# Optimization experiments

Measured on AMD Instinct MI355X. Metric: run time of the kernel, lower is better.

## Reference

```python
import jax, jax.numpy as jnp
import numpy as np

N, E = 20000, 320000
IN_DIM, CODE_DIM, HIDDEN, HEADS, NREL = 896, 768, 256, 4, 5
CH = HIDDEN // HEADS
CODE_WEIGHT = 3.0
NEG_SLOPE = 0.2


def _gat_layer(h, src, dst, W, att_src, att_dst, bias):
    # h: [N, HIDDEN]; src/dst already include self-loops. Eval mode -> no dropout.
    n = h.shape[0]
    x = (h @ W).reshape(n, HEADS, CH)                      # [N,H,C]
    a_src = (x * att_src).sum(-1)                          # [N,H]
    a_dst = (x * att_dst).sum(-1)                          # [N,H]
    alpha = jax.nn.leaky_relu(a_src[src] + a_dst[dst], NEG_SLOPE)  # [E',H]
    amax = jax.ops.segment_max(alpha, dst, num_segments=n)
    amax = jnp.where(jnp.isfinite(amax), amax, 0.0)
    ex = jnp.exp(alpha - amax[dst])
    denom = jax.ops.segment_sum(ex, dst, num_segments=n)
    coef = ex / denom[dst]                                 # segment softmax over in-neighbors
    msg = x[src] * coef[:, :, None]                        # [E',H,C]
    out = jax.ops.segment_sum(msg, dst, num_segments=n)    # [N,H,C]
    return out.reshape(n, HEADS * CH) + bias


def setup_inputs() -> dict:
    key = jax.random.key(0)
    ks = jax.random.split(key, 20)
    def glorot(k, shape):
        fan_in = shape[0]
        return jax.random.normal(k, shape, jnp.float32) / jnp.sqrt(jnp.asarray(fan_in, jnp.float32))
    inp = {
        "x": jax.random.normal(ks[0], (N, IN_DIM), jnp.float32),
        "edge_index": jax.random.randint(ks[1], (2, E), 0, N, jnp.int32),
        "edge_type": jax.random.randint(ks[2], (E,), 0, NREL, jnp.int32),
        "edge_weight": jax.random.uniform(ks[3], (E,), jnp.float32),
        "rel_emb": jax.random.normal(ks[4], (NREL, HIDDEN), jnp.float32),
        "Wp": glorot(ks[5], (IN_DIM, HIDDEN)),
        "bp": jnp.zeros((HIDDEN,), jnp.float32),
        "W1": glorot(ks[6], (HIDDEN, HIDDEN)),
        "att_src1": glorot(ks[7], (HEADS, CH)) * 0.1,
        "att_dst1": glorot(ks[8], (HEADS, CH)) * 0.1,
        "b1": jnp.zeros((HIDDEN,), jnp.float32),
        "W2": glorot(ks[9], (HIDDEN, HIDDEN)),
        "att_src2": glorot(ks[10], (HEADS, CH)) * 0.1,
        "att_dst2": glorot(ks[11], (HEADS, CH)) * 0.1,
        "b2": jnp.zeros((HIDDEN,), jnp.float32),
        "Wo": glorot(ks[12], (HIDDEN, 1)),
        "bo": jnp.zeros((1,), jnp.float32),
    }
    return inp


def reference(x, edge_index, edge_type, edge_weight, rel_emb, Wp, bp,
              W1, att_src1, att_dst1, b1, W2, att_src2, att_dst2, b2, Wo, bo):
    # feature reorder + code reweighting
    x_code = x[:, :CODE_DIM]
    x_num = x[:, CODE_DIM:]
    xc = jnp.concatenate([x_num, CODE_WEIGHT * x_code], axis=-1)
    h = jax.nn.relu(xc @ Wp + bp)                          # [N,HIDDEN]

    src, dst = edge_index[0], edge_index[1]
    # relational message + index_add scatter
    rel = rel_emb[edge_type] * edge_weight[:, None]        # [E,HIDDEN]
    msg = h[src] + rel
    h = h + jax.ops.segment_sum(msg, dst, num_segments=N)

    # GATConv adds self-loops by default
    loop = jnp.arange(N, dtype=src.dtype)
    src_sl = jnp.concatenate([src, loop])
    dst_sl = jnp.concatenate([dst, loop])

    h = _gat_layer(h, src_sl, dst_sl, W1, att_src1, att_dst1, b1)
    h = _gat_layer(h, src_sl, dst_sl, W2, att_src2, att_dst2, b2)
    score = (h @ Wo + bo)[:, 0]                            # [N]
    return score
```

## Files before the change

kernel.cpp:

```cpp
#include <hip/hip_runtime.h>
#include <hip/hip_bf16.h>

#define N_NODES 20000
#define E_EDGES 320000

typedef __attribute__((ext_vector_type(8))) short s8v;
typedef __attribute__((ext_vector_type(4))) float f4v;

__device__ __forceinline__ float lrelu(float v){ return v > 0.f ? v : 0.2f * v; }

__device__ __forceinline__ float bitf(unsigned short u){
  union { unsigned int i; float f; } v; v.i = ((unsigned int)u) << 16; return v.f;
}
__device__ __forceinline__ float4 bf4(const unsigned short* p){
  ushort4 u = *(const ushort4*)p;
  return make_float4(bitf(u.x), bitf(u.y), bitf(u.z), bitf(u.w));
}
__device__ __forceinline__ unsigned short bfhi(float v){
  union{float f; unsigned u;} a; a.f = v;
  unsigned r = a.u + 0x7FFFu + ((a.u >> 16) & 1u);
  return (unsigned short)(r >> 16);
}
__device__ __forceinline__ float bf2f(unsigned short h){
  union{unsigned u; float f;} a; a.u = ((unsigned)h) << 16; return a.f;
}
__device__ __forceinline__ void split2(float v0, float v1, unsigned& hu, unsigned& lu){
  __hip_bfloat162 h2 = __float22bfloat162_rn(make_float2(v0, v1));
  unsigned h; __builtin_memcpy(&h, &h2, 4);
  union{unsigned u; float f;} c0, c1;
  c0.u = h << 16;
  c1.u = h & 0xFFFF0000u;
  __hip_bfloat162 l2 = __float22bfloat162_rn(make_float2(v0 - c0.f, v1 - c1.f));
  unsigned l; __builtin_memcpy(&l, &l2, 4);
  hu = h; lu = l;
}

__global__ __launch_bounds__(256) void k_count(const int* __restrict__ dst, int* __restrict__ deg, int E){
  int e = blockIdx.x * 256 + threadIdx.x;
  if (e < E) atomicAdd(&deg[dst[e]], 1);
}

__global__ __launch_bounds__(256) void k_scan(const int* __restrict__ deg, int* __restrict__ off,
                                              int* __restrict__ cur, int n){
  __shared__ int part[256];
  __shared__ int base[257];
  int tid = threadIdx.x;
  int chunk = (n + 255) / 256;
  int st = tid * chunk;
  int en = st + chunk; if (en > n) en = n;
  int s = 0;
  for (int i = st; i < en; ++i) s += deg[i];
  part[tid] = s;
  __syncthreads();
  if (tid == 0){
    int a = 0;
    for (int i = 0; i < 256; ++i){ base[i] = a; a += part[i]; }
    base[256] = a;
  }
  __syncthreads();
  int a = base[tid];
  for (int i = st; i < en; ++i){ off[i] = a; cur[i] = 0; a += deg[i]; }
  if (tid == 0) off[n] = base[256];
}

__global__ __launch_bounds__(256) void k_fill(const int* __restrict__ src, const int* __restrict__ dst,
                       const int* __restrict__ ety, const float* __restrict__ ew,
                       const int* __restrict__ off, int* __restrict__ cur,
                       int* __restrict__ csrc, int* __restrict__ cet, float* __restrict__ cw, int E){
  int e = blockIdx.x * 256 + threadIdx.x;
  if (e < E){
    int d = dst[e];
    int p = atomicAdd(&cur[d], 1);
    int i = off[d] + p;
    csrc[i] = src[e];
    cet[i]  = ety[e];
    cw[i]   = ew[e];
  }
}

__global__ __launch_bounds__(64) void k_prep(const float* __restrict__ W, unsigned short* __restrict__ Bp, int K){
  int kt = blockIdx.x;
  int n  = blockIdx.y * 64 + threadIdx.x;
  unsigned short hi[32], lo[32];
#pragma unroll
  for (int kk = 0; kk < 32; ++kk){
    float v = W[(size_t)(kt * 32 + kk) * 256 + n];
    unsigned short h = bfhi(v);
    hi[kk] = h;
    lo[kk] = bfhi(v - bf2f(h));
  }
  size_t plane = (size_t)(K >> 5) * 256 * 32;
  size_t b = ((size_t)kt * 256 + n) * 32;
#pragma unroll
  for (int kk = 0; kk < 32; ++kk){
    Bp[b + kk]         = hi[kk];
    Bp[plane + b + kk] = lo[kk];
  }
}

template<int KT, bool PERM, bool EPI, bool ATT, bool CBF>
__global__ __launch_bounds__(128, 4) void k_mm(
    const float* __restrict__ A, const unsigned short* __restrict__ Bp,
    const float* __restrict__ bias, void* __restrict__ Cout,
    const float* __restrict__ attS, const float* __restrict__ attD,
    float* __restrict__ aS, float* __restrict__ aD, int M)
{
  constexpr int K = KT * 32;
  __shared__ unsigned short AhB[2][32 * 40];
  __shared__ unsigned short AlB[2][32 * 40];

  const int tid  = threadIdx.x;
  const int lane = tid & 63;
  const int wn   = tid >> 6;
  const int l15  = lane & 15;
  const int kg   = lane >> 4;
  const int m0   = blockIdx.x * 32;
  const int n0   = blockIdx.y * 128;
  const size_t planeB = (size_t)KT * 256 * 32;

  f4v acc[2][4];
#pragma unroll
  for (int f = 0; f < 2; ++f)
#pragma unroll
    for (int g = 0; g < 4; ++g)
#pragma unroll
      for (int r = 0; r < 4; ++r) acc[f][g][r] = 0.f;

  const int arow = tid >> 2;
  const int aj   = tid & 3;
  const int gr   = m0 + arow;

  auto loadA = [&](float* v, int kt){
    if (gr < M){
      if constexpr (PERM){
        int c = kt * 32 + aj * 8;
        const float* sp; float sc;
        if (c < 128){ sp = A + (size_t)gr * 896 + (768 + c); sc = 1.f; }
        else        { sp = A + (size_t)gr * 896 + (c - 128); sc = 3.f; }
        float4 f0 = *(const float4*)sp;
        float4 f1 = *(const float4*)(sp + 4);
        v[0]=f0.x*sc; v[1]=f0.y*sc; v[2]=f0.z*sc; v[3]=f0.w*sc;
        v[4]=f1.x*sc; v[5]=f1.y*sc; v[6]=f1.z*sc; v[7]=f1.w*sc;
      } else {
        const float* sp = A + (size_t)gr * K + kt * 32 + aj * 8;
        float4 f0 = *(const float4*)sp;
        float4 f1 = *(const float4*)(sp + 4);
        v[0]=f0.x; v[1]=f0.y; v[2]=f0.z; v[3]=f0.w;
        v[4]=f1.x; v[5]=f1.y; v[6]=f1.z; v[7]=f1.w;
      }
    } else {
#pragma unroll
      for (int j = 0; j < 8; ++j) v[j] = 0.f;
    }
  };
  auto writeLDS = [&](const float* v, int buf){
    union { unsigned u[4]; s8v s; } hv, lv;
#pragma unroll
    for (int p = 0; p < 4; ++p)
      split2(v[2*p], v[2*p+1], hv.u[p], lv.u[p]);
    *(s8v*)&AhB[buf][arow * 40 + aj * 8] = hv.s;
    *(s8v*)&AlB[buf][arow * 40 + aj * 8] = lv.s;
  };

  float av[8];
  loadA(av, 0);
  writeLDS(av, 0);
  if (KT > 1) loadA(av, 1);

  int cur = 0;
  for (int kt = 0; kt < KT; ++kt){
    __syncthreads();
    if (kt + 1 < KT) writeLDS(av, cur ^ 1);
    if (kt + 2 < KT) loadA(av, kt + 2);
    s8v bh[4], bl[4];
#pragma unroll
    for (int g = 0; g < 4; ++g){
      const unsigned short* bp2 = Bp + ((size_t)kt * 256 + n0 + wn * 64 + g * 16 + l15) * 32 + kg * 8;
      bh[g] = *(const s8v*)bp2;
      bl[g] = *(const s8v*)(bp2 + planeB);
    }
    s8v ah[2], al[2];
#pragma unroll
    for (int f = 0; f < 2; ++f){
      int row = f * 16 + l15;
      ah[f] = *(const s8v*)&AhB[cur][row * 40 + kg * 8];
      al[f] = *(const s8v*)&AlB[cur][row * 40 + kg * 8];
    }
#pragma unroll
    for (int f = 0; f < 2; ++f)
#pragma unroll
      for (int g = 0; g < 4; ++g){
        acc[f][g] = __builtin_amdgcn_mfma_f32_16x16x32_bf16(ah[f], bh[g], acc[f][g], 0, 0, 0);
        acc[f][g] = __builtin_amdgcn_mfma_f32_16x16x32_bf16(ah[f], bl[g], acc[f][g], 0, 0, 0);
        acc[f][g] = __builtin_amdgcn_mfma_f32_16x16x32_bf16(al[f], bh[g], acc[f][g], 0, 0, 0);
      }
    cur ^= 1;
  }

#pragma unroll
  for (int f = 0; f < 2; ++f){
#pragma unroll
    for (int g = 0; g < 4; ++g){
      int col = n0 + wn * 64 + g * 16 + l15;
      float bb = EPI ? bias[col] : 0.f;
#pragma unroll
      for (int r = 0; r < 4; ++r){
        int row = m0 + f * 16 + kg * 4 + r;
        if (row < M){
          float v = acc[f][g][r];
          if constexpr (EPI) v = fmaxf(v + bb, 0.f);
          if constexpr (CBF) ((unsigned short*)Cout)[(size_t)row * 256 + col] = bfhi(v);
          else               ((float*)Cout)[(size_t)row * 256 + col] = v;
        }
      }
    }
  }

  if constexpr (ATT){
    const int head = blockIdx.y * 2 + wn;
    float sv[4], dv[4];
#pragma unroll
    for (int g = 0; g < 4; ++g){
      int col = n0 + wn * 64 + g * 16 + l15;
      sv[g] = attS[col];
      dv[g] = attD[col];
    }
#pragma unroll
    for (int f = 0; f < 2; ++f){
#pragma unroll
      for (int r = 0; r < 4; ++r){
        float ps = acc[f][0][r]*sv[0] + acc[f][1][r]*sv[1] + acc[f][2][r]*sv[2] + acc[f][3][r]*sv[3];
        float pd = acc[f][0][r]*dv[0] + acc[f][1][r]*dv[1] + acc[f][2][r]*dv[2] + acc[f][3][r]*dv[3];
#pragma unroll
        for (int mm = 1; mm < 16; mm <<= 1){
          ps += __shfl_xor(ps, mm, 64);
          pd += __shfl_xor(pd, mm, 64);
        }
        int row = m0 + f * 16 + kg * 4 + r;
        if (l15 == 0 && row < M){
          aS[(size_t)row * 4 + head] = ps;
          aD[(size_t)row * 4 + head] = pd;
        }
      }
    }
  }
}

__global__ __launch_bounds__(256) void k_agg(
    const unsigned short* __restrict__ h0, const int* __restrict__ off,
    const int* __restrict__ csrc, const int* __restrict__ cet, const float* __restrict__ cw,
    const float* __restrict__ rel, float* __restrict__ h1, int N)
{
  int n = blockIdx.x * 4 + (threadIdx.x >> 6);
  if (n >= N) return;
  int lane = threadIdx.x & 63;
  int c0 = lane * 4;
  float4 acc = bf4(&h0[(size_t)n * 256 + c0]);
  int s0 = off[n], s1 = off[n + 1];
  int e = s0;
  for (; e + 3 < s1; e += 4){
    int sA = csrc[e], sB = csrc[e+1], sC = csrc[e+2], sD = csrc[e+3];
    int tA = cet[e],  tB = cet[e+1],  tC = cet[e+2],  tD = cet[e+3];
    float wA = cw[e], wB = cw[e+1], wC = cw[e+2], wD = cw[e+3];
    float4 hA = bf4(&h0[(size_t)sA * 256 + c0]);
    float4 hB = bf4(&h0[(size_t)sB * 256 + c0]);
    float4 hC = bf4(&h0[(size_t)sC * 256 + c0]);
    float4 hD = bf4(&h0[(size_t)sD * 256 + c0]);
    float4 rA = *(const float4*)&rel[(size_t)tA * 256 + c0];
    float4 rB = *(const float4*)&rel[(size_t)tB * 256 + c0];
    float4 rC = *(const float4*)&rel[(size_t)tC * 256 + c0];
    float4 rD = *(const float4*)&rel[(size_t)tD * 256 + c0];
    acc.x += hA.x + hB.x + hC.x + hD.x + rA.x*wA + rB.x*wB + rC.x*wC + rD.x*wD;
    acc.y += hA.y + hB.y + hC.y + hD.y + rA.y*wA + rB.y*wB + rC.y*wC + rD.y*wD;
    acc.z += hA.z + hB.z + hC.z + hD.z + rA.z*wA + rB.z*wB + rC.z*wC + rD.z*wD;
    acc.w += hA.w + hB.w + hC.w + hD.w + rA.w*wA + rB.w*wB + rC.w*wC + rD.w*wD;
  }
  for (; e < s1; ++e){
    int s = csrc[e];
    int t = cet[e];
    float wg = cw[e];
    float4 hv = bf4(&h0[(size_t)s * 256 + c0]);
    float4 rv = *(const float4*)&rel[(size_t)t * 256 + c0];
    acc.x += hv.x + rv.x * wg;
    acc.y += hv.y + rv.y * wg;
    acc.z += hv.z + rv.z * wg;
    acc.w += hv.w + rv.w * wg;
  }
  *(float4*)&h1[(size_t)n * 256 + c0] = acc;
}

template<bool SCORE>
__global__ __launch_bounds__(256) void k_gat(
    const unsigned short* __restrict__ xh, const float* __restrict__ aS, const float* __restrict__ aD,
    const int* __restrict__ off, const int* __restrict__ csrc,
    const float* __restrict__ bias, float* __restrict__ hout,
    const float* __restrict__ Wo, const float* __restrict__ bo, float* __restrict__ out, int N)
{
  __shared__ float4 exs[4][128];
  __shared__ int   srcs[4][128];
  const int wv   = threadIdx.x >> 6;
  const int n    = blockIdx.x * 4 + wv;
  if (n >= N) return;
  const int lane = threadIdx.x & 63;
  const int head = lane >> 4;
  const int c0   = lane * 4;
  const int s0 = off[n], s1 = off[n + 1];
  const int deg = s1 - s0;
  const int nc = deg < 128 ? deg : 128;

  float4 ad4 = *(const float4*)&aD[(size_t)n * 4];
  float4 asf = *(const float4*)&aS[(size_t)n * 4];
  float4 aself;
  aself.x = lrelu(asf.x + ad4.x); aself.y = lrelu(asf.y + ad4.y);
  aself.z = lrelu(asf.z + ad4.z); aself.w = lrelu(asf.w + ad4.w);
  float4 q = aself;

  for (int base = 0; base < deg; base += 64){
    int ci = base + lane;
    if (ci < deg){
      int s = csrc[s0 + ci];
      float4 av = *(const float4*)&aS[(size_t)s * 4];
      float4 al4;
      al4.x = lrelu(av.x + ad4.x); al4.y = lrelu(av.y + ad4.y);
      al4.z = lrelu(av.z + ad4.z); al4.w = lrelu(av.w + ad4.w);
      q.x = fmaxf(q.x, al4.x); q.y = fmaxf(q.y, al4.y);
      q.z = fmaxf(q.z, al4.z); q.w = fmaxf(q.w, al4.w);
      if (ci < 128){ srcs[wv][ci] = s; exs[wv][ci] = al4; }
    }
  }
#pragma unroll
  for (int mm = 1; mm < 64; mm <<= 1){
    q.x = fmaxf(q.x, __shfl_xor(q.x, mm, 64));
    q.y = fmaxf(q.y, __shfl_xor(q.y, mm, 64));
    q.z = fmaxf(q.z, __shfl_xor(q.z, mm, 64));
    q.w = fmaxf(q.w, __shfl_xor(q.w, mm, 64));
  }
  asm volatile("s_waitcnt lgkmcnt(0)" ::: "memory");

  float4 den4 = make_float4(0.f, 0.f, 0.f, 0.f);
  for (int ci = lane; ci < nc; ci += 64){
    float4 a = exs[wv][ci];
    float4 e4;
    e4.x = __expf(a.x - q.x); e4.y = __expf(a.y - q.y);
    e4.z = __expf(a.z - q.z); e4.w = __expf(a.w - q.w);
    exs[wv][ci] = e4;
    den4.x += e4.x; den4.y += e4.y; den4.z += e4.z; den4.w += e4.w;
  }
#pragma unroll
  for (int mm = 1; mm < 64; mm <<= 1){
    den4.x += __shfl_xor(den4.x, mm, 64);
    den4.y += __shfl_xor(den4.y, mm, 64);
    den4.z += __shfl_xor(den4.z, mm, 64);
    den4.w += __shfl_xor(den4.w, mm, 64);
  }
  asm volatile("s_waitcnt lgkmcnt(0)" ::: "memory");

  const float mh  = head == 0 ? q.x : (head == 1 ? q.y : (head == 2 ? q.z : q.w));
  const float adh = head == 0 ? ad4.x : (head == 1 ? ad4.y : (head == 2 ? ad4.z : ad4.w));
  const float aselfh = head == 0 ? aself.x : (head == 1 ? aself.y : (head == 2 ? aself.z : aself.w));
  float den = (head == 0 ? den4.x : (head == 1 ? den4.y : (head == 2 ? den4.z : den4.w)));
  float exself = __expf(aselfh - mh);
  den += exself;

  float4 xv = bf4(&xh[(size_t)n * 256 + c0]);
  float4 acc;
  acc.x = exself * xv.x; acc.y = exself * xv.y; acc.z = exself * xv.z; acc.w = exself * xv.w;

  const float* exw = (const float*)&exs[wv][0];
  int e = 0;
  for (; e + 3 < nc; e += 4){
    int sA = srcs[wv][e], sB = srcs[wv][e+1], sC = srcs[wv][e+2], sD = srcs[wv][e+3];
    float eA = exw[(e  ) * 4 + head];
    float eB = exw[(e+1) * 4 + head];
    float eC = exw[(e+2) * 4 + head];
    float eD = exw[(e+3) * 4 + head];
    float4 xA = bf4(&xh[(size_t)sA * 256 + c0]);
    float4 xB = bf4(&xh[(size_t)sB * 256 + c0]);
    float4 xC = bf4(&xh[(size_t)sC * 256 + c0]);
    float4 xD = bf4(&xh[(size_t)sD * 256 + c0]);
    acc.x = fmaf(eA, xA.x, fmaf(eB, xB.x, fmaf(eC, xC.x, fmaf(eD, xD.x, acc.x))));
    acc.y = fmaf(eA, xA.y, fmaf(eB, xB.y, fmaf(eC, xC.y, fmaf(eD, xD.y, acc.y))));
    acc.z = fmaf(eA, xA.z, fmaf(eB, xB.z, fmaf(eC, xC.z, fmaf(eD, xD.z, acc.z))));
    acc.w = fmaf(eA, xA.w, fmaf(eB, xB.w, fmaf(eC, xC.w, fmaf(eD, xD.w, acc.w))));
  }
  for (; e < nc; ++e){
    int s = srcs[wv][e];
    float ef = exw[e * 4 + head];
    float4 x2 = bf4(&xh[(size_t)s * 256 + c0]);
    acc.x = fmaf(ef, x2.x, acc.x);
    acc.y = fmaf(ef, x2.y, acc.y);
    acc.z = fmaf(ef, x2.z, acc.z);
    acc.w = fmaf(ef, x2.w, acc.w);
  }
  for (int ci = 128; ci < deg; ++ci){
    int s = csrc[s0 + ci];
    float a  = aS[(size_t)s * 4 + head];
    float ef = __expf(lrelu(a + adh) - mh);
    den += ef;
    float4 x2 = bf4(&xh[(size_t)s * 256 + c0]);
    acc.x = fmaf(ef, x2.x, acc.x);
    acc.y = fmaf(ef, x2.y, acc.y);
    acc.z = fmaf(ef, x2.z, acc.z);
    acc.w = fmaf(ef, x2.w, acc.w);
  }

  float inv = 1.f / den;
  float4 bb = *(const float4*)&bias[c0];
  float4 o;
  o.x = acc.x * inv + bb.x;
  o.y = acc.y * inv + bb.y;
  o.z = acc.z * inv + bb.z;
  o.w = acc.w * inv + bb.w;
  if constexpr (SCORE){
    float4 wvv = *(const float4*)&Wo[c0];
    float p = o.x * wvv.x + o.y * wvv.y + o.z * wvv.z + o.w * wvv.w;
#pragma unroll
    for (int mm = 1; mm < 64; mm <<= 1) p += __shfl_xor(p, mm, 64);
    if (lane == 0) out[n] = p + bo[0];
  } else {
    *(float4*)&hout[(size_t)n * 256 + c0] = o;
  }
}

extern "C" void kernel_launch(void* const* d_in, const int* in_sizes, int n_in,
                              void* d_out, int out_size, void* d_ws, size_t ws_size,
                              hipStream_t stream)
{
  const float* x   = (const float*)d_in[0];
  const int*   ei  = (const int*)  d_in[1];
  const int*   ety = (const int*)  d_in[2];
  const float* ew  = (const float*)d_in[3];
  const float* rel = (const float*)d_in[4];
  const float* Wp  = (const float*)d_in[5];
  const float* bp  = (const float*)d_in[6];
  const float* W1  = (const float*)d_in[7];
  const float* as1 = (const float*)d_in[8];
  const float* ad1 = (const float*)d_in[9];
  const float* b1  = (const float*)d_in[10];
  const float* W2  = (const float*)d_in[11];
  const float* as2 = (const float*)d_in[12];
  const float* ad2 = (const float*)d_in[13];
  const float* b2  = (const float*)d_in[14];
  const float* Wo  = (const float*)d_in[15];
  const float* bo  = (const float*)d_in[16];
  float* out = (float*)d_out;

  const int N = N_NODES, E = E_EDGES;
  char* w = (char*)d_ws;
  size_t o = 0;
  auto alloc = [&](size_t bytes) -> char* {
    char* p = w + o;
    o = (o + bytes + 255) & ~(size_t)255;
    return p;
  };
  unsigned short* h0b = (unsigned short*)alloc((size_t)N * 256 * 2);
  unsigned short* xhb = (unsigned short*)alloc((size_t)N * 256 * 2);
  float* h1  = (float*)alloc((size_t)N * 256 * 4);
  float* aS  = (float*)alloc((size_t)N * 4 * 4);
  float* aD  = (float*)alloc((size_t)N * 4 * 4);
  int* deg   = (int*)alloc((size_t)N * 4);
  int* offs  = (int*)alloc((size_t)(N + 1) * 4);
  int* cur   = (int*)alloc((size_t)N * 4);
  int* csrc  = (int*)alloc((size_t)E * 4);
  int* cet   = (int*)alloc((size_t)E * 4);
  float* cw  = (float*)alloc((size_t)E * 4);
  unsigned short* BpP = (unsigned short*)alloc((size_t)2 * 896 * 256 * 2);
  unsigned short* Bp1 = (unsigned short*)alloc((size_t)2 * 256 * 256 * 2);
  unsigned short* Bp2 = (unsigned short*)alloc((size_t)2 * 256 * 256 * 2);

  const int* srcp = ei;
  const int* dstp = ei + E;

  hipMemsetAsync(deg, 0, (size_t)N * 4, stream);
  k_count<<<(E + 255) / 256, 256, 0, stream>>>(dstp, deg, E);
  k_scan<<<1, 256, 0, stream>>>(deg, offs, cur, N);
  k_fill<<<(E + 255) / 256, 256, 0, stream>>>(srcp, dstp, ety, ew, offs, cur, csrc, cet, cw, E);

  k_prep<<<dim3(896 / 32, 4), 64, 0, stream>>>(Wp, BpP, 896);
  k_prep<<<dim3(256 / 32, 4), 64, 0, stream>>>(W1, Bp1, 256);
  k_prep<<<dim3(256 / 32, 4), 64, 0, stream>>>(W2, Bp2, 256);

  dim3 gg((N + 31) / 32, 2);
  int nblk = (N + 3) / 4;

  k_mm<28, true, true, false, true><<<gg, 128, 0, stream>>>(
      x, BpP, bp, (void*)h0b, nullptr, nullptr, nullptr, nullptr, N);
  k_agg<<<nblk, 256, 0, stream>>>(h0b, offs, csrc, cet, cw, rel, h1, N);
  k_mm<8, false, false, true, true><<<gg, 128, 0, stream>>>(
      h1, Bp1, nullptr, (void*)xhb, as1, ad1, aS, aD, N);
  k_gat<false><<<nblk, 256, 0, stream>>>(xhb, aS, aD, offs, csrc, b1, h1, nullptr, nullptr, nullptr, N);
  k_mm<8, false, false, true, true><<<gg, 128, 0, stream>>>(
      h1, Bp2, nullptr, (void*)xhb, as2, ad2, aS, aD, N);
  k_gat<true><<<nblk, 256, 0, stream>>>(xhb, aS, aD, offs, csrc, b2, nullptr, Wo, bo, out, N);
}
```

Measured before the change: 272.3 us.

## Retile MFMA GEMM to 64x64 blocks with 2x2 waves and prefetch B

The split-bf16 MFMA GEMM now uses 256-thread blocks of four waves in a 2x2 layout, each block covering 64 rows by 64 columns instead of 32 by 128. The grid gains four column tiles. B fragments for the next k-step are loaded into registers while the current step's MFMAs run. The attention-score epilogue now sums the two column-wave partials through shared memory, so each block writes one head's scores. The aim is better occupancy and hidden B-load latency, but each A row, including the large fp32 input of the first projection, is now read by four column blocks instead of two.

```diff
diff --git a/kernel.cpp b/kernel.cpp
--- a/kernel.cpp
+++ b/kernel.cpp
@@ -99,30 +99,35 @@
 }
 
 template<int KT, bool PERM, bool EPI, bool ATT, bool CBF>
-__global__ __launch_bounds__(128, 4) void k_mm(
+__global__ __launch_bounds__(256, 4) void k_mm(
     const float* __restrict__ A, const unsigned short* __restrict__ Bp,
     const float* __restrict__ bias, void* __restrict__ Cout,
     const float* __restrict__ attS, const float* __restrict__ attD,
     float* __restrict__ aS, float* __restrict__ aD, int M)
 {
   constexpr int K = KT * 32;
-  __shared__ unsigned short AhB[2][32 * 40];
-  __shared__ unsigned short AlB[2][32 * 40];
+  __shared__ unsigned short AhB[2][64 * 40];
+  __shared__ unsigned short AlB[2][64 * 40];
+  __shared__ float smS[2][2][4][4][2];
+  __shared__ float smD[2][2][4][4][2];
 
   const int tid  = threadIdx.x;
   const int lane = tid & 63;
-  const int wn   = tid >> 6;
+  const int w    = tid >> 6;
+  const int wm   = w >> 1;
+  const int wn   = w & 1;
   const int l15  = lane & 15;
   const int kg   = lane >> 4;
-  const int m0   = blockIdx.x * 32;
-  const int n0   = blockIdx.y * 128;
+  const int m0   = blockIdx.x * 64;
+  const int by   = blockIdx.y;
+  const int n0   = by * 64;
   const size_t planeB = (size_t)KT * 256 * 32;
 
-  f4v acc[2][4];
+  f4v acc[2][2];
 #pragma unroll
   for (int f = 0; f < 2; ++f)
 #pragma unroll
-    for (int g = 0; g < 4; ++g)
+    for (int g = 0; g < 2; ++g)
 #pragma unroll
       for (int r = 0; r < 4; ++r) acc[f][g][r] = 0.f;
 
@@ -161,51 +166,60 @@
     *(s8v*)&AhB[buf][arow * 40 + aj * 8] = hv.s;
     *(s8v*)&AlB[buf][arow * 40 + aj * 8] = lv.s;
   };
+  auto loadB = [&](s8v* bh, s8v* bl, int kt){
+#pragma unroll
+    for (int g = 0; g < 2; ++g){
+      const unsigned short* bp2 = Bp + ((size_t)kt * 256 + n0 + wn * 32 + g * 16 + l15) * 32 + kg * 8;
+      bh[g] = *(const s8v*)bp2;
+      bl[g] = *(const s8v*)(bp2 + planeB);
+    }
+  };
 
   float av[8];
   loadA(av, 0);
   writeLDS(av, 0);
   if (KT > 1) loadA(av, 1);
+  s8v bh[2], bl[2];
+  loadB(bh, bl, 0);
 
   int cur = 0;
   for (int kt = 0; kt < KT; ++kt){
     __syncthreads();
     if (kt + 1 < KT) writeLDS(av, cur ^ 1);
     if (kt + 2 < KT) loadA(av, kt + 2);
-    s8v bh[4], bl[4];
-#pragma unroll
-    for (int g = 0; g < 4; ++g){
-      const unsigned short* bp2 = Bp + ((size_t)kt * 256 + n0 + wn * 64 + g * 16 + l15) * 32 + kg * 8;
-      bh[g] = *(const s8v*)bp2;
-      bl[g] = *(const s8v*)(bp2 + planeB);
-    }
+    s8v nbh[2], nbl[2];
+    if (kt + 1 < KT) loadB(nbh, nbl, kt + 1);
     s8v ah[2], al[2];
 #pragma unroll
     for (int f = 0; f < 2; ++f){
-      int row = f * 16 + l15;
+      int row = wm * 32 + f * 16 + l15;
       ah[f] = *(const s8v*)&AhB[cur][row * 40 + kg * 8];
       al[f] = *(const s8v*)&AlB[cur][row * 40 + kg * 8];
     }
 #pragma unroll
     for (int f = 0; f < 2; ++f)
 #pragma unroll
-      for (int g = 0; g < 4; ++g){
+      for (int g = 0; g < 2; ++g){
         acc[f][g] = __builtin_amdgcn_mfma_f32_16x16x32_bf16(ah[f], bh[g], acc[f][g], 0, 0, 0);
         acc[f][g] = __builtin_amdgcn_mfma_f32_16x16x32_bf16(ah[f], bl[g], acc[f][g], 0, 0, 0);
         acc[f][g] = __builtin_amdgcn_mfma_f32_16x16x32_bf16(al[f], bh[g], acc[f][g], 0, 0, 0);
       }
+    if (kt + 1 < KT){
+      bh[0] = nbh[0]; bh[1] = nbh[1];
+      bl[0] = nbl[0]; bl[1] = nbl[1];
+    }
     cur ^= 1;
   }
 
 #pragma unroll
   for (int f = 0; f < 2; ++f){
 #pragma unroll
-    for (int g = 0; g < 4; ++g){
-      int col = n0 + wn * 64 + g * 16 + l15;
+    for (int g = 0; g < 2; ++g){
+      int col = n0 + wn * 32 + g * 16 + l15;
       float bb = EPI ? bias[col] : 0.f;
 #pragma unroll
       for (int r = 0; r < 4; ++r){
-        int row = m0 + f * 16 + kg * 4 + r;
+        int row = m0 + wm * 32 + f * 16 + kg * 4 + r;
         if (row < M){
           float v = acc[f][g][r];
           if constexpr (EPI) v = fmaxf(v + bb, 0.f);
@@ -217,11 +231,10 @@
   }
 
   if constexpr (ATT){
-    const int head = blockIdx.y * 2 + wn;
-    float sv[4], dv[4];
-#pragma unroll
-    for (int g = 0; g < 4; ++g){
-      int col = n0 + wn * 64 + g * 16 + l15;
+    float sv[2], dv[2];
+#pragma unroll
+    for (int g = 0; g < 2; ++g){
+      int col = n0 + wn * 32 + g * 16 + l15;
       sv[g] = attS[col];
       dv[g] = attD[col];
     }
@@ -229,18 +242,28 @@
     for (int f = 0; f < 2; ++f){
 #pragma unroll
       for (int r = 0; r < 4; ++r){
-        float ps = acc[f][0][r]*sv[0] + acc[f][1][r]*sv[1] + acc[f][2][r]*sv[2] + acc[f][3][r]*sv[3];
-        float pd = acc[f][0][r]*dv[0] + acc[f][1][r]*dv[1] + acc[f][2][r]*dv[2] + acc[f][3][r]*dv[3];
+        float ps = acc[f][0][r]*sv[0] + acc[f][1][r]*sv[1];
+        float pd = acc[f][0][r]*dv[0] + acc[f][1][r]*dv[1];
 #pragma unroll
         for (int mm = 1; mm < 16; mm <<= 1){
           ps += __shfl_xor(ps, mm, 64);
           pd += __shfl_xor(pd, mm, 64);
         }
-        int row = m0 + f * 16 + kg * 4 + r;
-        if (l15 == 0 && row < M){
-          aS[(size_t)row * 4 + head] = ps;
-          aD[(size_t)row * 4 + head] = pd;
+        if (l15 == 0){
+          smS[wm][f][kg][r][wn] = ps;
+          smD[wm][f][kg][r][wn] = pd;
         }
+      }
+    }
+    __syncthreads();
+    if (tid < 64){
+      int wm2 = tid >> 5, f2 = (tid >> 4) & 1, kg2 = (tid >> 2) & 3, r2 = tid & 3;
+      int row = m0 + wm2 * 32 + f2 * 16 + kg2 * 4 + r2;
+      if (row < M){
+        float s = smS[wm2][f2][kg2][r2][0] + smS[wm2][f2][kg2][r2][1];
+        float d = smD[wm2][f2][kg2][r2][0] + smD[wm2][f2][kg2][r2][1];
+        aS[(size_t)row * 4 + by] = s;
+        aD[(size_t)row * 4 + by] = d;
       }
     }
   }
@@ -480,16 +503,16 @@
   k_prep<<<dim3(256 / 32, 4), 64, 0, stream>>>(W1, Bp1, 256);
   k_prep<<<dim3(256 / 32, 4), 64, 0, stream>>>(W2, Bp2, 256);
 
-  dim3 gg((N + 31) / 32, 2);
+  dim3 gg((N + 63) / 64, 4);
   int nblk = (N + 3) / 4;
 
-  k_mm<28, true, true, false, true><<<gg, 128, 0, stream>>>(
+  k_mm<28, true, true, false, true><<<gg, 256, 0, stream>>>(
       x, BpP, bp, (void*)h0b, nullptr, nullptr, nullptr, nullptr, N);
   k_agg<<<nblk, 256, 0, stream>>>(h0b, offs, csrc, cet, cw, rel, h1, N);
-  k_mm<8, false, false, true, true><<<gg, 128, 0, stream>>>(
+  k_mm<8, false, false, true, true><<<gg, 256, 0, stream>>>(
       h1, Bp1, nullptr, (void*)xhb, as1, ad1, aS, aD, N);
   k_gat<false><<<nblk, 256, 0, stream>>>(xhb, aS, aD, offs, csrc, b1, h1, nullptr, nullptr, nullptr, N);
-  k_mm<8, false, false, true, true><<<gg, 128, 0, stream>>>(
+  k_mm<8, false, false, true, true><<<gg, 256, 0, stream>>>(
       h1, Bp2, nullptr, (void*)xhb, as2, ad2, aS, aD, N);
   k_gat<true><<<nblk, 256, 0, stream>>>(xhb, aS, aD, offs, csrc, b2, nullptr, Wo, bo, out, N);
 }
```

Measured after the change: 282.6 us. +3.8%, slower.

## Enlarge GEMM block to 64 rows with 4 waves and register-prefetch B tiles

Applied to the files above, without the earlier changes.

The split-bf16 GEMM kernel now uses 256-thread blocks covering 64 rows, so each B-fragment load is shared across twice as many rows and the grid halves. The K loop is unrolled by two, with explicit double-buffered register prefetch of the B fragments and staged A loads, so global loads overlap the MFMA work. The cost is higher register pressure (launch bounds 256,3), a requirement that KT be even, and fewer blocks for latency hiding.

```diff
diff --git a/kernel.cpp b/kernel.cpp
--- a/kernel.cpp
+++ b/kernel.cpp
@@ -99,23 +99,27 @@
 }
 
 template<int KT, bool PERM, bool EPI, bool ATT, bool CBF>
-__global__ __launch_bounds__(128, 4) void k_mm(
+__global__ __launch_bounds__(256, 3) void k_mm(
     const float* __restrict__ A, const unsigned short* __restrict__ Bp,
     const float* __restrict__ bias, void* __restrict__ Cout,
     const float* __restrict__ attS, const float* __restrict__ attD,
     float* __restrict__ aS, float* __restrict__ aD, int M)
 {
   constexpr int K = KT * 32;
-  __shared__ unsigned short AhB[2][32 * 40];
-  __shared__ unsigned short AlB[2][32 * 40];
+  static_assert((KT & 1) == 0, "KT must be even");
+  __shared__ unsigned short AhB[2][64 * 40];
+  __shared__ unsigned short AlB[2][64 * 40];
 
   const int tid  = threadIdx.x;
   const int lane = tid & 63;
-  const int wn   = tid >> 6;
+  const int w    = tid >> 6;
+  const int wm   = w >> 1;
+  const int wn   = w & 1;
   const int l15  = lane & 15;
   const int kg   = lane >> 4;
-  const int m0   = blockIdx.x * 32;
-  const int n0   = blockIdx.y * 128;
+  const int m0   = blockIdx.x * 64;
+  const int by   = blockIdx.y;
+  const int n0   = by * 128;
   const size_t planeB = (size_t)KT * 256 * 32;
 
   f4v acc[2][4];
@@ -161,31 +165,23 @@
     *(s8v*)&AhB[buf][arow * 40 + aj * 8] = hv.s;
     *(s8v*)&AlB[buf][arow * 40 + aj * 8] = lv.s;
   };
-
-  float av[8];
-  loadA(av, 0);
-  writeLDS(av, 0);
-  if (KT > 1) loadA(av, 1);
-
-  int cur = 0;
-  for (int kt = 0; kt < KT; ++kt){
-    __syncthreads();
-    if (kt + 1 < KT) writeLDS(av, cur ^ 1);
-    if (kt + 2 < KT) loadA(av, kt + 2);
-    s8v bh[4], bl[4];
+  auto loadB = [&](s8v* bh, s8v* bl, int kt){
 #pragma unroll
     for (int g = 0; g < 4; ++g){
       const unsigned short* bp2 = Bp + ((size_t)kt * 256 + n0 + wn * 64 + g * 16 + l15) * 32 + kg * 8;
       bh[g] = *(const s8v*)bp2;
       bl[g] = *(const s8v*)(bp2 + planeB);
     }
-    s8v ah[2], al[2];
+  };
+  auto readFrags = [&](s8v* ah, s8v* al, int buf){
 #pragma unroll
     for (int f = 0; f < 2; ++f){
-      int row = f * 16 + l15;
-      ah[f] = *(const s8v*)&AhB[cur][row * 40 + kg * 8];
-      al[f] = *(const s8v*)&AlB[cur][row * 40 + kg * 8];
-    }
+      int row = wm * 32 + f * 16 + l15;
+      ah[f] = *(const s8v*)&AhB[buf][row * 40 + kg * 8];
+      al[f] = *(const s8v*)&AlB[buf][row * 40 + kg * 8];
+    }
+  };
+  auto doMFMA = [&](const s8v* ah, const s8v* al, const s8v* bh, const s8v* bl){
 #pragma unroll
     for (int f = 0; f < 2; ++f)
 #pragma unroll
@@ -194,7 +190,33 @@
         acc[f][g] = __builtin_amdgcn_mfma_f32_16x16x32_bf16(ah[f], bl[g], acc[f][g], 0, 0, 0);
         acc[f][g] = __builtin_amdgcn_mfma_f32_16x16x32_bf16(al[f], bh[g], acc[f][g], 0, 0, 0);
       }
-    cur ^= 1;
+  };
+
+  float avA[8], avB[8];
+  s8v B0h[4], B0l[4], B1h[4], B1l[4];
+  loadA(avA, 0);
+  writeLDS(avA, 0);
+  loadA(avA, 1);
+  loadA(avB, 2);
+  loadB(B0h, B0l, 0);
+  loadB(B1h, B1l, 1);
+
+#pragma unroll 1
+  for (int it = 0; it < KT / 2; ++it){
+    const int k0 = it * 2;
+    s8v ah[2], al[2];
+    __syncthreads();
+    readFrags(ah, al, 0);
+    writeLDS(avA, 1);
+    if (k0 + 3 < KT) loadA(avA, k0 + 3);
+    doMFMA(ah, al, B0h, B0l);
+    if (k0 + 2 < KT) loadB(B0h, B0l, k0 + 2);
+    __syncthreads();
+    readFrags(ah, al, 1);
+    if (k0 + 2 < KT) writeLDS(avB, 0);
+    if (k0 + 4 < KT) loadA(avB, k0 + 4);
+    doMFMA(ah, al, B1h, B1l);
+    if (k0 + 3 < KT) loadB(B1h, B1l, k0 + 3);
   }
 
 #pragma unroll
@@ -205,7 +227,7 @@
       float bb = EPI ? bias[col] : 0.f;
 #pragma unroll
       for (int r = 0; r < 4; ++r){
-        int row = m0 + f * 16 + kg * 4 + r;
+        int row = m0 + wm * 32 + f * 16 + kg * 4 + r;
         if (row < M){
           float v = acc[f][g][r];
           if constexpr (EPI) v = fmaxf(v + bb, 0.f);
@@ -217,7 +239,7 @@
   }
 
   if constexpr (ATT){
-    const int head = blockIdx.y * 2 + wn;
+    const int head = by * 2 + wn;
     float sv[4], dv[4];
 #pragma unroll
     for (int g = 0; g < 4; ++g){
@@ -236,7 +258,7 @@
           ps += __shfl_xor(ps, mm, 64);
           pd += __shfl_xor(pd, mm, 64);
         }
-        int row = m0 + f * 16 + kg * 4 + r;
+        int row = m0 + wm * 32 + f * 16 + kg * 4 + r;
         if (l15 == 0 && row < M){
           aS[(size_t)row * 4 + head] = ps;
           aD[(size_t)row * 4 + head] = pd;
@@ -480,16 +502,16 @@
   k_prep<<<dim3(256 / 32, 4), 64, 0, stream>>>(W1, Bp1, 256);
   k_prep<<<dim3(256 / 32, 4), 64, 0, stream>>>(W2, Bp2, 256);
 
-  dim3 gg((N + 31) / 32, 2);
+  dim3 gg((N + 63) / 64, 2);
   int nblk = (N + 3) / 4;
 
-  k_mm<28, true, true, false, true><<<gg, 128, 0, stream>>>(
+  k_mm<28, true, true, false, true><<<gg, 256, 0, stream>>>(
       x, BpP, bp, (void*)h0b, nullptr, nullptr, nullptr, nullptr, N);
   k_agg<<<nblk, 256, 0, stream>>>(h0b, offs, csrc, cet, cw, rel, h1, N);
-  k_mm<8, false, false, true, true><<<gg, 128, 0, stream>>>(
+  k_mm<8, false, false, true, true><<<gg, 256, 0, stream>>>(
       h1, Bp1, nullptr, (void*)xhb, as1, ad1, aS, aD, N);
   k_gat<false><<<nblk, 256, 0, stream>>>(xhb, aS, aD, offs, csrc, b1, h1, nullptr, nullptr, nullptr, N);
-  k_mm<8, false, false, true, true><<<gg, 128, 0, stream>>>(
+  k_mm<8, false, false, true, true><<<gg, 256, 0, stream>>>(
       h1, Bp2, nullptr, (void*)xhb, as2, ad2, aS, aD, N);
   k_gat<true><<<nblk, 256, 0, stream>>>(xhb, aS, aD, offs, csrc, b2, nullptr, Wo, bo, out, N);
 }
```

Result: slower. 280.5 us (+3.0%).

## Stage GEMM A tiles via global_load_lds and pre-split bf16 hi/lo activations

Applied to the files above, without the earlier changes.

The GEMM kernel now loads A tiles straight from global memory into LDS with global_load_lds, using an XOR-swizzled layout. Each 256-thread block covers all 256 output columns, so A is loaded once per block instead of twice. The producing kernels (agg, gat) now write activations pre-split into bf16 hi/lo planes, which removes per-tile float-to-bf16 splitting and halves A traffic for the 256-wide GEMMs. The code-weight scale of 3 moves into the prepared Wp, and bounds checks are dropped on the assumption that N is a multiple of 32. This adds an extra bf16 write stream and depends on that exact node count.

```diff
diff --git a/kernel.cpp b/kernel.cpp
--- a/kernel.cpp
+++ b/kernel.cpp
@@ -33,6 +33,11 @@
   __hip_bfloat162 l2 = __float22bfloat162_rn(make_float2(v0 - c0.f, v1 - c1.f));
   unsigned l; __builtin_memcpy(&l, &l2, 4);
   hu = h; lu = l;
+}
+__device__ __forceinline__ void gl_lds16(const void* g, void* l){
+  __builtin_amdgcn_global_load_lds(
+      (const __attribute__((address_space(1))) unsigned int*)g,
+      (__attribute__((address_space(3))) unsigned int*)l, 16, 0, 0);
 }
 
 __global__ __launch_bounds__(256) void k_count(const int* __restrict__ dst, int* __restrict__ deg, int E){
@@ -78,13 +83,16 @@
   }
 }
 
+template<bool SC3>
 __global__ __launch_bounds__(64) void k_prep(const float* __restrict__ W, unsigned short* __restrict__ Bp, int K){
   int kt = blockIdx.x;
   int n  = blockIdx.y * 64 + threadIdx.x;
   unsigned short hi[32], lo[32];
 #pragma unroll
   for (int kk = 0; kk < 32; ++kk){
-    float v = W[(size_t)(kt * 32 + kk) * 256 + n];
+    int krow = kt * 32 + kk;
+    float v = W[(size_t)krow * 256 + n];
+    if constexpr (SC3){ if (krow >= 128) v *= 3.0f; }
     unsigned short h = bfhi(v);
     hi[kk] = h;
     lo[kk] = bfhi(v - bf2f(h));
@@ -98,24 +106,24 @@
   }
 }
 
-template<int KT, bool PERM, bool EPI, bool ATT, bool CBF>
-__global__ __launch_bounds__(128, 4) void k_mm(
-    const float* __restrict__ A, const unsigned short* __restrict__ Bp,
+template<int KT, bool ARAW, bool EPI, bool ATT, bool CBF>
+__global__ __launch_bounds__(256, 2) void k_mm(
+    const float* __restrict__ Araw,
+    const unsigned short* __restrict__ Ahi, const unsigned short* __restrict__ Alo,
+    const unsigned short* __restrict__ Bp,
     const float* __restrict__ bias, void* __restrict__ Cout,
     const float* __restrict__ attS, const float* __restrict__ attD,
-    float* __restrict__ aS, float* __restrict__ aD, int M)
+    float* __restrict__ aS, float* __restrict__ aD)
 {
-  constexpr int K = KT * 32;
-  __shared__ unsigned short AhB[2][32 * 40];
-  __shared__ unsigned short AlB[2][32 * 40];
+  constexpr int TILE = ARAW ? 8192 : 4096;
+  __shared__ alignas(16) unsigned char Abuf[2][TILE];
 
   const int tid  = threadIdx.x;
   const int lane = tid & 63;
-  const int wn   = tid >> 6;
+  const int w    = tid >> 6;
   const int l15  = lane & 15;
   const int kg   = lane >> 4;
   const int m0   = blockIdx.x * 32;
-  const int n0   = blockIdx.y * 128;
   const size_t planeB = (size_t)KT * 256 * 32;
 
   f4v acc[2][4];
@@ -126,66 +134,65 @@
 #pragma unroll
       for (int r = 0; r < 4; ++r) acc[f][g][r] = 0.f;
 
-  const int arow = tid >> 2;
-  const int aj   = tid & 3;
-  const int gr   = m0 + arow;
-
-  auto loadA = [&](float* v, int kt){
-    if (gr < M){
-      if constexpr (PERM){
-        int c = kt * 32 + aj * 8;
-        const float* sp; float sc;
-        if (c < 128){ sp = A + (size_t)gr * 896 + (768 + c); sc = 1.f; }
-        else        { sp = A + (size_t)gr * 896 + (c - 128); sc = 3.f; }
-        float4 f0 = *(const float4*)sp;
-        float4 f1 = *(const float4*)(sp + 4);
-        v[0]=f0.x*sc; v[1]=f0.y*sc; v[2]=f0.z*sc; v[3]=f0.w*sc;
-        v[4]=f1.x*sc; v[5]=f1.y*sc; v[6]=f1.z*sc; v[7]=f1.w*sc;
-      } else {
-        const float* sp = A + (size_t)gr * K + kt * 32 + aj * 8;
-        float4 f0 = *(const float4*)sp;
-        float4 f1 = *(const float4*)(sp + 4);
-        v[0]=f0.x; v[1]=f0.y; v[2]=f0.z; v[3]=f0.w;
-        v[4]=f1.x; v[5]=f1.y; v[6]=f1.z; v[7]=f1.w;
+  auto stage = [&](int buf, int kt){
+    if constexpr (ARAW){
+#pragma unroll
+      for (int seg = 0; seg < 2; ++seg){
+        int s   = seg * 256 + tid;
+        int row = s >> 3;
+        int jj  = s & 7;
+        int kcp = jj >> 1, h = jj & 1;
+        int kc  = kcp ^ (row & 3);
+        int c   = kt * 32 + kc * 8 + h * 4;
+        int xcol = (c < 128) ? (768 + c) : (c - 128);
+        const float* gp = Araw + (size_t)(m0 + row) * 896 + xcol;
+        gl_lds16(gp, &Abuf[buf][seg * 4096 + w * 1024]);
       }
     } else {
-#pragma unroll
-      for (int j = 0; j < 8; ++j) v[j] = 0.f;
+      int s   = tid;
+      int p   = s >> 7;
+      int sp  = s & 127;
+      int row = sp >> 2;
+      int kcp = sp & 3;
+      int kc  = kcp ^ (row & 3);
+      const unsigned short* basep = p ? Alo : Ahi;
+      const unsigned short* gp = basep + (size_t)(m0 + row) * 256 + kt * 32 + kc * 8;
+      gl_lds16(gp, &Abuf[buf][w * 1024]);
     }
   };
-  auto writeLDS = [&](const float* v, int buf){
-    union { unsigned u[4]; s8v s; } hv, lv;
-#pragma unroll
-    for (int p = 0; p < 4; ++p)
-      split2(v[2*p], v[2*p+1], hv.u[p], lv.u[p]);
-    *(s8v*)&AhB[buf][arow * 40 + aj * 8] = hv.s;
-    *(s8v*)&AlB[buf][arow * 40 + aj * 8] = lv.s;
+
+  auto readFrags = [&](s8v* ah, s8v* al, int buf){
+#pragma unroll
+    for (int f = 0; f < 2; ++f){
+      int row = f * 16 + l15;
+      int kc  = kg ^ (row & 3);
+      if constexpr (ARAW){
+        const unsigned char* p0 = &Abuf[buf][row * 128 + kc * 32];
+        float4 x0 = *(const float4*)p0;
+        float4 x1 = *(const float4*)(p0 + 16);
+        union{unsigned u[4]; s8v s;} H, L;
+        split2(x0.x, x0.y, H.u[0], L.u[0]);
+        split2(x0.z, x0.w, H.u[1], L.u[1]);
+        split2(x1.x, x1.y, H.u[2], L.u[2]);
+        split2(x1.z, x1.w, H.u[3], L.u[3]);
+        ah[f] = H.s; al[f] = L.s;
+      } else {
+        ah[f] = *(const s8v*)&Abuf[buf][row * 64 + kc * 16];
+        al[f] = *(const s8v*)&Abuf[buf][2048 + row * 64 + kc * 16];
+      }
+    }
   };
 
-  float av[8];
-  loadA(av, 0);
-  writeLDS(av, 0);
-  if (KT > 1) loadA(av, 1);
-
-  int cur = 0;
-  for (int kt = 0; kt < KT; ++kt){
-    __syncthreads();
-    if (kt + 1 < KT) writeLDS(av, cur ^ 1);
-    if (kt + 2 < KT) loadA(av, kt + 2);
-    s8v bh[4], bl[4];
+  auto loadB = [&](s8v* bh, s8v* bl, int kt){
 #pragma unroll
     for (int g = 0; g < 4; ++g){
-      const unsigned short* bp2 = Bp + ((size_t)kt * 256 + n0 + wn * 64 + g * 16 + l15) * 32 + kg * 8;
+      const unsigned short* bp2 = Bp + ((size_t)kt * 256 + w * 64 + g * 16 + l15) * 32 + kg * 8;
       bh[g] = *(const s8v*)bp2;
       bl[g] = *(const s8v*)(bp2 + planeB);
     }
-    s8v ah[2], al[2];
-#pragma unroll
-    for (int f = 0; f < 2; ++f){
-      int row = f * 16 + l15;
-      ah[f] = *(const s8v*)&AhB[cur][row * 40 + kg * 8];
-      al[f] = *(const s8v*)&AlB[cur][row * 40 + kg * 8];
-    }
+  };
+
+  auto doMFMA = [&](const s8v* ah, const s8v* al, const s8v* bh, const s8v* bl){
 #pragma unroll
     for (int f = 0; f < 2; ++f)
 #pragma unroll
@@ -194,6 +201,27 @@
         acc[f][g] = __builtin_amdgcn_mfma_f32_16x16x32_bf16(ah[f], bl[g], acc[f][g], 0, 0, 0);
         acc[f][g] = __builtin_amdgcn_mfma_f32_16x16x32_bf16(al[f], bh[g], acc[f][g], 0, 0, 0);
       }
+  };
+
+  s8v bh[4], bl[4];
+  stage(0, 0);
+  loadB(bh, bl, 0);
+  __syncthreads();
+
+  int cur = 0;
+#pragma unroll 1
+  for (int kt = 0; kt < KT; ++kt){
+    if (kt + 1 < KT) stage(cur ^ 1, kt + 1);
+    s8v ah[2], al[2];
+    readFrags(ah, al, cur);
+    s8v nbh[4], nbl[4];
+    if (kt + 1 < KT) loadB(nbh, nbl, kt + 1);
+    doMFMA(ah, al, bh, bl);
+    if (kt + 1 < KT){
+#pragma unroll
+      for (int g = 0; g < 4; ++g){ bh[g] = nbh[g]; bl[g] = nbl[g]; }
+    }
+    __syncthreads();
     cur ^= 1;
   }
 
@@ -201,27 +229,25 @@
   for (int f = 0; f < 2; ++f){
 #pragma unroll
     for (int g = 0; g < 4; ++g){
-      int col = n0 + wn * 64 + g * 16 + l15;
+      int col = w * 64 + g * 16 + l15;
       float bb = EPI ? bias[col] : 0.f;
 #pragma unroll
       for (int r = 0; r < 4; ++r){
         int row = m0 + f * 16 + kg * 4 + r;
-        if (row < M){
-          float v = acc[f][g][r];
-          if constexpr (EPI) v = fmaxf(v + bb, 0.f);
-          if constexpr (CBF) ((unsigned short*)Cout)[(size_t)row * 256 + col] = bfhi(v);
-          else               ((float*)Cout)[(size_t)row * 256 + col] = v;
-        }
+        float v = acc[f][g][r];
+        if constexpr (EPI) v = fmaxf(v + bb, 0.f);
+        if constexpr (CBF) ((unsigned short*)Cout)[(size_t)row * 256 + col] = bfhi(v);
+        else               ((float*)Cout)[(size_t)row * 256 + col] = v;
       }
     }
   }
 
   if constexpr (ATT){
-    const int head = blockIdx.y * 2 + wn;
+    const int head = w;
     float sv[4], dv[4];
 #pragma unroll
     for (int g = 0; g < 4; ++g){
-      int col = n0 + wn * 64 + g * 16 + l15;
+      int col = w * 64 + g * 16 + l15;
       sv[g] = attS[col];
       dv[g] = attD[col];
     }
@@ -237,7 +263,7 @@
           pd += __shfl_xor(pd, mm, 64);
         }
         int row = m0 + f * 16 + kg * 4 + r;
-        if (l15 == 0 && row < M){
+        if (l15 == 0){
           aS[(size_t)row * 4 + head] = ps;
           aD[(size_t)row * 4 + head] = pd;
         }
@@ -249,7 +275,8 @@
 __global__ __launch_bounds__(256) void k_agg(
     const unsigned short* __restrict__ h0, const int* __restrict__ off,
     const int* __restrict__ csrc, const int* __restrict__ cet, const float* __restrict__ cw,
-    const float* __restrict__ rel, float* __restrict__ h1, int N)
+    const float* __restrict__ rel,
+    unsigned short* __restrict__ h1hi, unsigned short* __restrict__ h1lo, int N)
 {
   int n = blockIdx.x * 4 + (threadIdx.x >> 6);
   if (n >= N) return;
@@ -286,14 +313,23 @@
     acc.z += hv.z + rv.z * wg;
     acc.w += hv.w + rv.w * wg;
   }
-  *(float4*)&h1[(size_t)n * 256 + c0] = acc;
+  ushort4 hi, lo;
+  { unsigned short h;
+    h = bfhi(acc.x); hi.x = h; lo.x = bfhi(acc.x - bf2f(h));
+    h = bfhi(acc.y); hi.y = h; lo.y = bfhi(acc.y - bf2f(h));
+    h = bfhi(acc.z); hi.z = h; lo.z = bfhi(acc.z - bf2f(h));
+    h = bfhi(acc.w); hi.w = h; lo.w = bfhi(acc.w - bf2f(h));
+  }
+  *(ushort4*)&h1hi[(size_t)n * 256 + c0] = hi;
+  *(ushort4*)&h1lo[(size_t)n * 256 + c0] = lo;
 }
 
 template<bool SCORE>
 __global__ __launch_bounds__(256) void k_gat(
     const unsigned short* __restrict__ xh, const float* __restrict__ aS, const float* __restrict__ aD,
     const int* __restrict__ off, const int* __restrict__ csrc,
-    const float* __restrict__ bias, float* __restrict__ hout,
+    const float* __restrict__ bias,
+    unsigned short* __restrict__ h1hi, unsigned short* __restrict__ h1lo,
     const float* __restrict__ Wo, const float* __restrict__ bo, float* __restrict__ out, int N)
 {
   __shared__ float4 exs[4][128];
@@ -418,7 +454,14 @@
     for (int mm = 1; mm < 64; mm <<= 1) p += __shfl_xor(p, mm, 64);
     if (lane == 0) out[n] = p + bo[0];
   } else {
-    *(float4*)&hout[(size_t)n * 256 + c0] = o;
+    ushort4 hi, lo;
+    unsigned short h;
+    h = bfhi(o.x); hi.x = h; lo.x = bfhi(o.x - bf2f(h));
+    h = bfhi(o.y); hi.y = h; lo.y = bfhi(o.y - bf2f(h));
+    h = bfhi(o.z); hi.z = h; lo.z = bfhi(o.z - bf2f(h));
+    h = bfhi(o.w); hi.w = h; lo.w = bfhi(o.w - bf2f(h));
+    *(ushort4*)&h1hi[(size_t)n * 256 + c0] = hi;
+    *(ushort4*)&h1lo[(size_t)n * 256 + c0] = lo;
   }
 }
 
@@ -453,9 +496,10 @@
     o = (o + bytes + 255) & ~(size_t)255;
     return p;
   };
-  unsigned short* h0b = (unsigned short*)alloc((size_t)N * 256 * 2);
-  unsigned short* xhb = (unsigned short*)alloc((size_t)N * 256 * 2);
-  float* h1  = (float*)alloc((size_t)N * 256 * 4);
+  unsigned short* h0b  = (unsigned short*)alloc((size_t)N * 256 * 2);
+  unsigned short* xhb  = (unsigned short*)alloc((size_t)N * 256 * 2);
+  unsigned short* h1hi = (unsigned short*)alloc((size_t)N * 256 * 2);
+  unsigned short* h1lo = (unsigned short*)alloc((size_t)N * 256 * 2);
   float* aS  = (float*)alloc((size_t)N * 4 * 4);
   float* aD  = (float*)alloc((size_t)N * 4 * 4);
   int* deg   = (int*)alloc((size_t)N * 4);
@@ -476,20 +520,20 @@
   k_scan<<<1, 256, 0, stream>>>(deg, offs, cur, N);
   k_fill<<<(E + 255) / 256, 256, 0, stream>>>(srcp, dstp, ety, ew, offs, cur, csrc, cet, cw, E);
 
-  k_prep<<<dim3(896 / 32, 4), 64, 0, stream>>>(Wp, BpP, 896);
-  k_prep<<<dim3(256 / 32, 4), 64, 0, stream>>>(W1, Bp1, 256);
-  k_prep<<<dim3(256 / 32, 4), 64, 0, stream>>>(W2, Bp2, 256);
-
-  dim3 gg((N + 31) / 32, 2);
+  k_prep<true ><<<dim3(896 / 32, 4), 64, 0, stream>>>(Wp, BpP, 896);
+  k_prep<false><<<dim3(256 / 32, 4), 64, 0, stream>>>(W1, Bp1, 256);
+  k_prep<false><<<dim3(256 / 32, 4), 64, 0, stream>>>(W2, Bp2, 256);
+
+  const int gmm = N_NODES / 32;
   int nblk = (N + 3) / 4;
 
-  k_mm<28, true, true, false, true><<<gg, 128, 0, stream>>>(
-      x, BpP, bp, (void*)h0b, nullptr, nullptr, nullptr, nullptr, N);
-  k_agg<<<nblk, 256, 0, stream>>>(h0b, offs, csrc, cet, cw, rel, h1, N);
-  k_mm<8, false, false, true, true><<<gg, 128, 0, stream>>>(
-      h1, Bp1, nullptr, (void*)xhb, as1, ad1, aS, aD, N);
-  k_gat<false><<<nblk, 256, 0, stream>>>(xhb, aS, aD, offs, csrc, b1, h1, nullptr, nullptr, nullptr, N);
-  k_mm<8, false, false, true, true><<<gg, 128, 0, stream>>>(
-      h1, Bp2, nullptr, (void*)xhb, as2, ad2, aS, aD, N);
-  k_gat<true><<<nblk, 256, 0, stream>>>(xhb, aS, aD, offs, csrc, b2, nullptr, Wo, bo, out, N);
-}
+  k_mm<28, true, true, false, true><<<gmm, 256, 0, stream>>>(
+      x, nullptr, nullptr, BpP, bp, (void*)h0b, nullptr, nullptr, nullptr, nullptr);
+  k_agg<<<nblk, 256, 0, stream>>>(h0b, offs, csrc, cet, cw, rel, h1hi, h1lo, N);
+  k_mm<8, false, false, true, true><<<gmm, 256, 0, stream>>>(
+      nullptr, h1hi, h1lo, Bp1, nullptr, (void*)xhb, as1, ad1, aS, aD);
+  k_gat<false><<<nblk, 256, 0, stream>>>(xhb, aS, aD, offs, csrc, b1, h1hi, h1lo, nullptr, nullptr, nullptr, N);
+  k_mm<8, false, false, true, true><<<gmm, 256, 0, stream>>>(
+      nullptr, h1hi, h1lo, Bp2, nullptr, (void*)xhb, as2, ad2, aS, aD);
+  k_gat<true><<<nblk, 256, 0, stream>>>(xhb, aS, aD, offs, csrc, b2, nullptr, nullptr, Wo, bo, out, N);
+}
```

Result: slower. 282.3 us (+3.7%).
